# Kernel tuning notes

Hardware: AMD Instinct MI355X
Metric: run time of the kernel (lower is better)

## Reference

```python
import jax, jax.numpy as jnp
import numpy as np

EMBED_DIM = 768
NUM_HEADS = 12
HEAD_DIM = EMBED_DIM // NUM_HEADS
SCALE = HEAD_DIM ** -0.5


def setup_inputs() -> dict:
    key = jax.random.key(0)
    ks = jax.random.split(key, 5)
    B, T, D = 8, 1024, EMBED_DIM
    lim_qkv = (1.0 / D) ** 0.5
    x = jax.random.normal(ks[0], (B, T, D), dtype=jnp.float32)
    W_qkv = jax.random.uniform(ks[1], (D, 3 * D), dtype=jnp.float32, minval=-lim_qkv, maxval=lim_qkv)
    b_qkv = jax.random.uniform(ks[2], (3 * D,), dtype=jnp.float32, minval=-lim_qkv, maxval=lim_qkv)
    W_proj = jax.random.uniform(ks[3], (D, D), dtype=jnp.float32, minval=-lim_qkv, maxval=lim_qkv)
    b_proj = jax.random.uniform(ks[4], (D,), dtype=jnp.float32, minval=-lim_qkv, maxval=lim_qkv)
    return {"x": x, "W_qkv": W_qkv, "b_qkv": b_qkv, "W_proj": W_proj, "b_proj": b_proj}


def reference(x, W_qkv, b_qkv, W_proj, b_proj):
    B, T, D = x.shape
    H, Hd = NUM_HEADS, HEAD_DIM
    # fused QKV projection: [B,T,3D] -> [3,B,H,T,Hd]
    qkv = (x @ W_qkv + b_qkv).reshape(B, T, 3, H, Hd).transpose(2, 0, 3, 1, 4)
    q, k, v = qkv[0], qkv[1], qkv[2]
    attn = jax.nn.softmax(jnp.einsum("bhqd,bhkd->bhqk", q, k) * SCALE, axis=-1)
    out = jnp.einsum("bhqk,bhkd->bhqd", attn, v)  # [B,H,T,Hd]
    out = out.transpose(0, 2, 1, 3).reshape(B, T, D)
    return out @ W_proj + b_proj
```

## Files before the change

### kernel.cpp

```cpp
#include <hip/hip_runtime.h>
#include <hip/hip_bf16.h>
#include <stdint.h>

#define NB 8
#define NT 1024
#define ND 768
#define NH 12

static constexpr float QSCALE = 0.125f * 1.44269504f;

typedef __bf16 bf16x8 __attribute__((ext_vector_type(8)));
typedef float f32x4 __attribute__((ext_vector_type(4)));
typedef unsigned short u16;

__device__ __forceinline__ u16 f2b(float f) {
  union { float f; uint32_t u; } c; c.f = f;
  uint32_t u = c.u;
  u += 0x7fffu + ((u >> 16) & 1u);
  return (u16)(u >> 16);
}

__device__ __forceinline__ uint32_t pk2(float a, float b) {
  __hip_bfloat162 p = __float22bfloat162_rn(make_float2(a, b));
  return *reinterpret_cast<uint32_t*>(&p);
}

__device__ __forceinline__ float exp2_raw(float x) {
  float y;
  asm("v_exp_f32 %0, %1" : "=v"(y) : "v"(x));
  return y;
}

__device__ __forceinline__ void gload16(const void* g, void* l) {
  __builtin_amdgcn_global_load_lds(
      (const __attribute__((address_space(1))) void*)g,
      (__attribute__((address_space(3))) void*)l, 16, 0, 0);
}

__global__ void k_cast(const float* __restrict__ in, u16* __restrict__ out, int n4) {
  int i = blockIdx.x * blockDim.x + threadIdx.x;
  if (i >= n4) return;
  float4 v = reinterpret_cast<const float4*>(in)[i];
  ushort4 o;
  o.x = f2b(v.x); o.y = f2b(v.y); o.z = f2b(v.z); o.w = f2b(v.w);
  reinterpret_cast<ushort4*>(out)[i] = o;
}

__global__ void k_tcast(const float* __restrict__ in, u16* __restrict__ out, int R, int C) {
  __shared__ float tile[32][33];
  int c0 = blockIdx.x * 32, r0 = blockIdx.y * 32;
  int tx = threadIdx.x & 31, ty = threadIdx.x >> 5;
  #pragma unroll
  for (int rr = ty; rr < 32; rr += 8)
    tile[rr][tx] = in[(size_t)(r0 + rr) * C + c0 + tx];
  __syncthreads();
  #pragma unroll
  for (int cc = ty; cc < 32; cc += 8)
    out[(size_t)(c0 + cc) * R + r0 + tx] = f2b(tile[tx][cc]);
}

__launch_bounds__(256, 4)
__global__ void k_gemm_qkv(const u16* __restrict__ A, const u16* __restrict__ Bt,
                           const float* __restrict__ bias,
                           u16* __restrict__ Qg, u16* __restrict__ KV)
{
  __shared__ u16 Al[128 * 64];
  __shared__ u16 Bl[128 * 64];
  const int tid = threadIdx.x, lane = tid & 63, wv = tid >> 6;
  const int g = lane >> 4, r = lane & 15;
  const int wm = (wv >> 1) * 64, wn = (wv & 1) * 64;
  const int bid = blockIdx.x + blockIdx.y * 18;
  const int swz = (bid & 7) * 144 + (bid >> 3);
  const int m0 = (swz / 18) * 128, n0 = (swz % 18) * 128;
  const int srow = lane >> 3;
  const int scolsw = ((lane & 7) ^ (lane >> 3)) * 8;
  f32x4 acc[4][4] = {};
  for (int k0 = 0; k0 < ND; k0 += 64) {
    __syncthreads();
    #pragma unroll
    for (int i = 0; i < 4; ++i) {
      int c = wv * 4 + i;
      gload16(&A[(size_t)(m0 + c * 8 + srow) * ND + k0 + scolsw], &Al[c * 512]);
      gload16(&Bt[(size_t)(n0 + c * 8 + srow) * ND + k0 + scolsw], &Bl[c * 512]);
    }
    __syncthreads();
    #pragma unroll
    for (int kk = 0; kk < 2; ++kk) {
      bf16x8 af[4], bfr[4];
      #pragma unroll
      for (int mf = 0; mf < 4; ++mf)
        af[mf] = *reinterpret_cast<const bf16x8*>(
            &Al[(wm + mf * 16 + r) * 64 + (((kk << 2) + g) ^ (r & 7)) * 8]);
      #pragma unroll
      for (int nf = 0; nf < 4; ++nf)
        bfr[nf] = *reinterpret_cast<const bf16x8*>(
            &Bl[(wn + nf * 16 + r) * 64 + (((kk << 2) + g) ^ (r & 7)) * 8]);
      #pragma unroll
      for (int mf = 0; mf < 4; ++mf)
        #pragma unroll
        for (int nf = 0; nf < 4; ++nf)
          acc[mf][nf] = __builtin_amdgcn_mfma_f32_16x16x32_bf16(af[mf], bfr[nf], acc[mf][nf], 0, 0, 0);
    }
  }
  #pragma unroll
  for (int mf = 0; mf < 4; ++mf)
    #pragma unroll
    for (int nf = 0; nf < 4; ++nf) {
      int col = n0 + wn + nf * 16 + r;
      int which = col / ND, c = col - which * ND;
      int h = c >> 6, hd = c & 63;
      int row0 = m0 + wm + mf * 16 + 4 * g;
      int bb = row0 >> 10, t0 = row0 & 1023;
      size_t bh = (size_t)bb * NH + h;
      float b = bias[col];
      if (which == 0) {
        #pragma unroll
        for (int jj = 0; jj < 4; ++jj)
          Qg[(bh * NT + t0 + jj) * 64 + hd] = f2b((acc[mf][nf][jj] + b) * QSCALE);
      } else if (which == 1) {
        int kt = t0 >> 6, nfk = (t0 >> 4) & 3, rk0 = t0 & 15;
        int kk = hd >> 5, ghd = (hd >> 3) & 3, e = hd & 7;
        size_t base = (bh * 16 + kt) * 8192 + (size_t)(nfk * 2 + kk) * 512 + e;
        #pragma unroll
        for (int jj = 0; jj < 4; ++jj)
          KV[base + (ghd * 16 + rk0 + jj) * 8] = f2b(acc[mf][nf][jj] + b);
      } else {
        int kt = t0 >> 6, tl0 = t0 & 63;
        int ks = tl0 >> 5, gv = (tl0 >> 3) & 3, e0 = tl0 & 7;
        int hf = hd >> 4, rv = hd & 15;
        size_t base = (bh * 16 + kt) * 8192 + 4096 +
                      (size_t)(hf * 2 + ks) * 512 + (gv * 16 + rv) * 8 + e0;
        ushort4 o;
        o.x = f2b(acc[mf][nf][0] + b);
        o.y = f2b(acc[mf][nf][1] + b);
        o.z = f2b(acc[mf][nf][2] + b);
        o.w = f2b(acc[mf][nf][3] + b);
        *reinterpret_cast<ushort4*>(&KV[base]) = o;
      }
    }
}

__launch_bounds__(256, 4)
__global__ void k_attn(const u16* __restrict__ Qg, const u16* __restrict__ KV,
                       u16* __restrict__ Ob)
{
  __shared__ u16 kv[2][8192];
  __shared__ u16 Pl[4][1024];
  const int tid = threadIdx.x, lane = tid & 63, wv = tid >> 6;
  const int g = lane >> 4, r = lane & 15;
  const int bh = blockIdx.x;
  const int qt = blockIdx.y;
  const int bb = bh / NH, h = bh - bb * NH;
  const u16* Qb = Qg + (size_t)bh * NT * 64;
  const u16* kvb = KV + (size_t)bh * 16 * 8192;

  bf16x8 qf[2][2];
  #pragma unroll
  for (int mf = 0; mf < 2; ++mf)
    #pragma unroll
    for (int kk = 0; kk < 2; ++kk) {
      int qrow = qt * 128 + wv * 32 + mf * 16 + r;
      qf[mf][kk] = *reinterpret_cast<const bf16x8*>(&Qb[(size_t)qrow * 64 + kk * 32 + g * 8]);
    }

  bf16x8 ones;
  #pragma unroll
  for (int i = 0; i < 8; ++i) ones[i] = (__bf16)1.0f;

  f32x4 lacc[2] = {};
  f32x4 oacc[2][4] = {};

  const u16* srcbase = kvb + wv * 512 + lane * 8;
  #pragma unroll
  for (int i = 0; i < 4; ++i)
    gload16(srcbase + i * 2048, &kv[0][wv * 512 + i * 2048]);
  asm volatile("s_waitcnt vmcnt(0)" ::: "memory");
  __syncthreads();

  for (int kt = 0; kt < 16; ++kt) {
    const int cur = kt & 1;
    if (kt < 15) {
      const u16* src = srcbase + (size_t)(kt + 1) * 8192;
      #pragma unroll
      for (int i = 0; i < 4; ++i)
        gload16(src + i * 2048, &kv[cur ^ 1][wv * 512 + i * 2048]);
    }
    const u16* Kb = kv[cur];
    const u16* Vb = kv[cur] + 4096;
    u16* Pw = Pl[wv];

    f32x4 st[2][4] = {};
    __builtin_amdgcn_s_setprio(1);
    #pragma unroll
    for (int kk = 0; kk < 2; ++kk) {
      bf16x8 kf[4];
      #pragma unroll
      for (int nf = 0; nf < 4; ++nf)
        kf[nf] = *reinterpret_cast<const bf16x8*>(&Kb[(nf * 2 + kk) * 512 + lane * 8]);
      #pragma unroll
      for (int mf = 0; mf < 2; ++mf)
        #pragma unroll
        for (int nf = 0; nf < 4; ++nf)
          st[mf][nf] = __builtin_amdgcn_mfma_f32_16x16x32_bf16(kf[nf], qf[mf][kk], st[mf][nf], 0, 0, 0);
    }
    __builtin_amdgcn_s_setprio(0);

    #pragma unroll
    for (int mf = 0; mf < 2; ++mf)
      #pragma unroll
      for (int nf = 0; nf < 4; ++nf)
        #pragma unroll
        for (int jj = 0; jj < 4; ++jj)
          st[mf][nf][jj] = exp2_raw(st[mf][nf][jj]);

    #pragma unroll
    for (int ks = 0; ks < 2; ++ks) {
      #pragma unroll
      for (int mf = 0; mf < 2; ++mf)
        #pragma unroll
        for (int u = 0; u < 2; ++u) {
          uint2 w;
          w.x = pk2(st[mf][2 * ks + u][0], st[mf][2 * ks + u][1]);
          w.y = pk2(st[mf][2 * ks + u][2], st[mf][2 * ks + u][3]);
          int gp = u * 2 + (g >> 1);
          *reinterpret_cast<uint2*>(&Pw[mf * 512 + (gp * 16 + r) * 8 + (g & 1) * 4]) = w;
        }
      bf16x8 pf[2], vf[4];
      #pragma unroll
      for (int mf = 0; mf < 2; ++mf)
        pf[mf] = *reinterpret_cast<const bf16x8*>(&Pw[mf * 512 + lane * 8]);
      #pragma unroll
      for (int hf = 0; hf < 4; ++hf)
        vf[hf] = *reinterpret_cast<const bf16x8*>(&Vb[(hf * 2 + ks) * 512 + lane * 8]);
      __builtin_amdgcn_s_setprio(1);
      #pragma unroll
      for (int mf = 0; mf < 2; ++mf) {
        #pragma unroll
        for (int hf = 0; hf < 4; ++hf)
          oacc[mf][hf] = __builtin_amdgcn_mfma_f32_16x16x32_bf16(vf[hf], pf[mf], oacc[mf][hf], 0, 0, 0);
        lacc[mf] = __builtin_amdgcn_mfma_f32_16x16x32_bf16(ones, pf[mf], lacc[mf], 0, 0, 0);
      }
      __builtin_amdgcn_s_setprio(0);
    }

    asm volatile("s_waitcnt vmcnt(0)" ::: "memory");
    __syncthreads();
  }

  #pragma unroll
  for (int mf = 0; mf < 2; ++mf) {
    float inv = 1.f / lacc[mf][0];
    int row = qt * 128 + wv * 32 + mf * 16 + r;
    #pragma unroll
    for (int hf = 0; hf < 4; ++hf) {
      uint2 w;
      w.x = pk2(oacc[mf][hf][0] * inv, oacc[mf][hf][1] * inv);
      w.y = pk2(oacc[mf][hf][2] * inv, oacc[mf][hf][3] * inv);
      *reinterpret_cast<uint2*>(&Ob[((size_t)(bb * NT + row)) * ND + h * 64 + hf * 16 + 4 * g]) = w;
    }
  }
}

__launch_bounds__(256, 4)
__global__ void k_gemm_proj(const u16* __restrict__ A, const u16* __restrict__ Bt,
                            const float* __restrict__ bias, float* __restrict__ out)
{
  __shared__ u16 Al[128 * 32];
  __shared__ u16 Bl[64 * 32];
  const int tid = threadIdx.x, lane = tid & 63, wv = tid >> 6;
  const int g = lane >> 4, r = lane & 15;
  const int wm = (wv >> 1) * 64, wn = (wv & 1) * 32;
  const int bid = blockIdx.x + blockIdx.y * 12;
  const int swz = (bid & 7) * 96 + (bid >> 3);
  const int m0 = (swz / 12) * 128, n0 = (swz % 12) * 64;
  const int srow = lane >> 2;
  const int scol = (lane & 3) * 8;
  f32x4 acc[4][2] = {};
  for (int k0 = 0; k0 < ND; k0 += 32) {
    __syncthreads();
    #pragma unroll
    for (int i = 0; i < 2; ++i) {
      int c = wv * 2 + i;
      gload16(&A[(size_t)(m0 + c * 16 + srow) * ND + k0 + scol], &Al[c * 512]);
    }
    gload16(&Bt[(size_t)(n0 + wv * 16 + srow) * ND + k0 + scol], &Bl[wv * 512]);
    __syncthreads();
    bf16x8 af[4], bfr[2];
    #pragma unroll
    for (int mf = 0; mf < 4; ++mf)
      af[mf] = *reinterpret_cast<const bf16x8*>(&Al[(wm + mf * 16 + r) * 32 + g * 8]);
    #pragma unroll
    for (int nf = 0; nf < 2; ++nf)
      bfr[nf] = *reinterpret_cast<const bf16x8*>(&Bl[(wn + nf * 16 + r) * 32 + g * 8]);
    #pragma unroll
    for (int mf = 0; mf < 4; ++mf)
      #pragma unroll
      for (int nf = 0; nf < 2; ++nf)
        acc[mf][nf] = __builtin_amdgcn_mfma_f32_16x16x32_bf16(af[mf], bfr[nf], acc[mf][nf], 0, 0, 0);
  }
  #pragma unroll
  for (int mf = 0; mf < 4; ++mf)
    #pragma unroll
    for (int nf = 0; nf < 2; ++nf) {
      int col = n0 + wn + nf * 16 + r;
      float b = bias[col];
      #pragma unroll
      for (int jj = 0; jj < 4; ++jj) {
        int row = m0 + wm + mf * 16 + 4 * g + jj;
        out[(size_t)row * ND + col] = acc[mf][nf][jj] + b;
      }
    }
}

extern "C" void kernel_launch(void* const* d_in, const int* in_sizes, int n_in,
                              void* d_out, int out_size, void* d_ws, size_t ws_size,
                              hipStream_t stream)
{
  const float* x     = (const float*)d_in[0];
  const float* Wqkv  = (const float*)d_in[1];
  const float* bqkv  = (const float*)d_in[2];
  const float* Wproj = (const float*)d_in[3];
  const float* bproj = (const float*)d_in[4];
  float* out = (float*)d_out;

  char* ws = (char*)d_ws;
  u16* xb  = (u16*)(ws + 0);
  u16* wqt = (u16*)(ws + 12582912);
  u16* wpt = (u16*)(ws + 16121856);
  u16* Qg  = (u16*)(ws + 17301504);
  u16* KV  = (u16*)(ws + 29884416);
  u16* Ob  = (u16*)(ws + 55050240);

  k_cast<<<dim3((8192 * 768 / 4 + 255) / 256), dim3(256), 0, stream>>>(x, xb, 8192 * 768 / 4);
  k_tcast<<<dim3(2304 / 32, 768 / 32), dim3(256), 0, stream>>>(Wqkv, wqt, 768, 2304);
  k_tcast<<<dim3(768 / 32, 768 / 32), dim3(256), 0, stream>>>(Wproj, wpt, 768, 768);
  k_gemm_qkv<<<dim3(2304 / 128, 8192 / 128), dim3(256), 0, stream>>>(xb, wqt, bqkv, Qg, KV);
  k_attn<<<dim3(96, 8), dim3(256), 0, stream>>>(Qg, KV, Ob);
  k_gemm_proj<<<dim3(768 / 64, 8192 / 128), dim3(256), 0, stream>>>(Ob, wpt, bproj, out);
}
```

Baseline: 111.1 us.

## Use 256x256 double-buffered tiles with prefetch in QKV GEMM

The QKV GEMM moves to 512-thread blocks computing 256x256 output tiles, with LDS double buffering so the next K-slice loads while MFMAs run on the current one. Wave priority is raised around the MFMA blocks. The intent is more data reuse per LDS load and hiding global load latency behind compute. The cost is a large LDS footprint and one block per CU, which reduces latency hiding across blocks.

Result: slower. 132.2 us (+19.0%).

```diff
diff --git a/kernel.cpp b/kernel.cpp
--- a/kernel.cpp
+++ b/kernel.cpp
@@ -59,71 +59,104 @@
     out[(size_t)(c0 + cc) * R + r0 + tx] = f2b(tile[tx][cc]);
 }
 
-__launch_bounds__(256, 4)
+__launch_bounds__(512, 1)
 __global__ void k_gemm_qkv(const u16* __restrict__ A, const u16* __restrict__ Bt,
                            const float* __restrict__ bias,
                            u16* __restrict__ Qg, u16* __restrict__ KV)
 {
-  __shared__ u16 Al[128 * 64];
-  __shared__ u16 Bl[128 * 64];
+  __shared__ u16 Al[2][2][8192];
+  __shared__ u16 Bl[2][2][8192];
   const int tid = threadIdx.x, lane = tid & 63, wv = tid >> 6;
   const int g = lane >> 4, r = lane & 15;
-  const int wm = (wv >> 1) * 64, wn = (wv & 1) * 64;
-  const int bid = blockIdx.x + blockIdx.y * 18;
-  const int swz = (bid & 7) * 144 + (bid >> 3);
-  const int m0 = (swz / 18) * 128, n0 = (swz % 18) * 128;
+  const int ah = wv >> 2;
+  const int bq = wv & 3;
+  const int bhl = bq >> 1, bo = (bq & 1) * 64;
+  const int bid = blockIdx.x + blockIdx.y * 9;
+  const int swz = (bid & 7) * 36 + (bid >> 3);
+  const int m0 = (swz / 9) * 256, n0 = (swz % 9) * 256;
   const int srow = lane >> 3;
   const int scolsw = ((lane & 7) ^ (lane >> 3)) * 8;
-  f32x4 acc[4][4] = {};
-  for (int k0 = 0; k0 < ND; k0 += 64) {
-    __syncthreads();
-    #pragma unroll
-    for (int i = 0; i < 4; ++i) {
-      int c = wv * 4 + i;
-      gload16(&A[(size_t)(m0 + c * 8 + srow) * ND + k0 + scolsw], &Al[c * 512]);
-      gload16(&Bt[(size_t)(n0 + c * 8 + srow) * ND + k0 + scolsw], &Bl[c * 512]);
-    }
-    __syncthreads();
-    #pragma unroll
-    for (int kk = 0; kk < 2; ++kk) {
-      bf16x8 af[4], bfr[4];
-      #pragma unroll
-      for (int mf = 0; mf < 4; ++mf)
-        af[mf] = *reinterpret_cast<const bf16x8*>(
-            &Al[(wm + mf * 16 + r) * 64 + (((kk << 2) + g) ^ (r & 7)) * 8]);
-      #pragma unroll
-      for (int nf = 0; nf < 4; ++nf)
-        bfr[nf] = *reinterpret_cast<const bf16x8*>(
-            &Bl[(wn + nf * 16 + r) * 64 + (((kk << 2) + g) ^ (r & 7)) * 8]);
-      #pragma unroll
-      for (int mf = 0; mf < 4; ++mf)
-        #pragma unroll
-        for (int nf = 0; nf < 4; ++nf)
-          acc[mf][nf] = __builtin_amdgcn_mfma_f32_16x16x32_bf16(af[mf], bfr[nf], acc[mf][nf], 0, 0, 0);
-    }
+  const int c0 = wv * 2, c1 = wv * 2 + 1;
+
+  #define STG(G, rowbase, k0, dst)                                                      \
+    do {                                                                                \
+      gload16(&(G)[(size_t)((rowbase) + c0 * 8 + srow) * ND + (k0) + scolsw], &(dst)[c0 * 512]); \
+      gload16(&(G)[(size_t)((rowbase) + c1 * 8 + srow) * ND + (k0) + scolsw], &(dst)[c1 * 512]); \
+    } while (0)
+
+  f32x4 acc[8][4] = {};
+
+  STG(A, m0, 0, Al[0][0]);        STG(Bt, n0, 0, Bl[0][0]);
+  STG(A, m0 + 128, 0, Al[0][1]);  STG(Bt, n0 + 128, 0, Bl[0][1]);
+  STG(A, m0, 64, Al[1][0]);       STG(Bt, n0, 64, Bl[1][0]);
+  STG(A, m0 + 128, 64, Al[1][1]); STG(Bt, n0 + 128, 64, Bl[1][1]);
+  asm volatile("s_waitcnt vmcnt(8)" ::: "memory");
+  __builtin_amdgcn_s_barrier();
+
+  for (int t = 0; t < 12; ++t) {
+    const int kb = t & 1;
+    if (t >= 1 && t <= 10) {
+      const int nb = kb ^ 1;
+      const int k1 = (t + 1) * 64;
+      STG(A, m0, k1, Al[nb][0]);        STG(Bt, n0, k1, Bl[nb][0]);
+      STG(A, m0 + 128, k1, Al[nb][1]);  STG(Bt, n0 + 128, k1, Bl[nb][1]);
+    }
+    const u16* Ah = Al[kb][ah];
+    const u16* Bh = Bl[kb][bhl];
+    #pragma unroll
+    for (int p = 0; p < 4; ++p) {
+      const int mh = p & 1, nh = p >> 1;
+      bf16x8 af[4][2], bfr[2][2];
+      #pragma unroll
+      for (int kk = 0; kk < 2; ++kk) {
+        #pragma unroll
+        for (int q = 0; q < 4; ++q)
+          af[q][kk] = *reinterpret_cast<const bf16x8*>(
+              &Ah[(mh * 64 + q * 16 + r) * 64 + (((kk << 2) + g) ^ (r & 7)) * 8]);
+        #pragma unroll
+        for (int u = 0; u < 2; ++u)
+          bfr[u][kk] = *reinterpret_cast<const bf16x8*>(
+              &Bh[(bo + (nh * 2 + u) * 16 + r) * 64 + (((kk << 2) + g) ^ (r & 7)) * 8]);
+      }
+      __builtin_amdgcn_s_setprio(1);
+      #pragma unroll
+      for (int kk = 0; kk < 2; ++kk)
+        #pragma unroll
+        for (int q = 0; q < 4; ++q)
+          #pragma unroll
+          for (int u = 0; u < 2; ++u)
+            acc[mh * 4 + q][nh * 2 + u] = __builtin_amdgcn_mfma_f32_16x16x32_bf16(
+                af[q][kk], bfr[u][kk], acc[mh * 4 + q][nh * 2 + u], 0, 0, 0);
+      __builtin_amdgcn_s_setprio(0);
+    }
+    asm volatile("s_waitcnt lgkmcnt(0)" ::: "memory");
+    asm volatile("s_waitcnt vmcnt(0)" ::: "memory");
+    __builtin_amdgcn_s_barrier();
   }
-  #pragma unroll
-  for (int mf = 0; mf < 4; ++mf)
+  #undef STG
+
+  #pragma unroll
+  for (int amf = 0; amf < 8; ++amf)
     #pragma unroll
     for (int nf = 0; nf < 4; ++nf) {
-      int col = n0 + wn + nf * 16 + r;
+      int col = n0 + bq * 64 + nf * 16 + r;
       int which = col / ND, c = col - which * ND;
       int h = c >> 6, hd = c & 63;
-      int row0 = m0 + wm + mf * 16 + 4 * g;
+      int row0 = m0 + ah * 128 + amf * 16 + 4 * g;
       int bb = row0 >> 10, t0 = row0 & 1023;
       size_t bh = (size_t)bb * NH + h;
       float b = bias[col];
       if (which == 0) {
         #pragma unroll
         for (int jj = 0; jj < 4; ++jj)
-          Qg[(bh * NT + t0 + jj) * 64 + hd] = f2b((acc[mf][nf][jj] + b) * QSCALE);
+          Qg[(bh * NT + t0 + jj) * 64 + hd] = f2b((acc[amf][nf][jj] + b) * QSCALE);
       } else if (which == 1) {
         int kt = t0 >> 6, nfk = (t0 >> 4) & 3, rk0 = t0 & 15;
         int kk = hd >> 5, ghd = (hd >> 3) & 3, e = hd & 7;
         size_t base = (bh * 16 + kt) * 8192 + (size_t)(nfk * 2 + kk) * 512 + e;
         #pragma unroll
         for (int jj = 0; jj < 4; ++jj)
-          KV[base + (ghd * 16 + rk0 + jj) * 8] = f2b(acc[mf][nf][jj] + b);
+          KV[base + (ghd * 16 + rk0 + jj) * 8] = f2b(acc[amf][nf][jj] + b);
       } else {
         int kt = t0 >> 6, tl0 = t0 & 63;
         int ks = tl0 >> 5, gv = (tl0 >> 3) & 3, e0 = tl0 & 7;
@@ -131,10 +164,10 @@
         size_t base = (bh * 16 + kt) * 8192 + 4096 +
                       (size_t)(hf * 2 + ks) * 512 + (gv * 16 + rv) * 8 + e0;
         ushort4 o;
-        o.x = f2b(acc[mf][nf][0] + b);
-        o.y = f2b(acc[mf][nf][1] + b);
-        o.z = f2b(acc[mf][nf][2] + b);
-        o.w = f2b(acc[mf][nf][3] + b);
+        o.x = f2b(acc[amf][nf][0] + b);
+        o.y = f2b(acc[amf][nf][1] + b);
+        o.z = f2b(acc[amf][nf][2] + b);
+        o.w = f2b(acc[amf][nf][3] + b);
         *reinterpret_cast<ushort4*>(&KV[base]) = o;
       }
     }
@@ -334,7 +367,7 @@
   k_cast<<<dim3((8192 * 768 / 4 + 255) / 256), dim3(256), 0, stream>>>(x, xb, 8192 * 768 / 4);
   k_tcast<<<dim3(2304 / 32, 768 / 32), dim3(256), 0, stream>>>(Wqkv, wqt, 768, 2304);
   k_tcast<<<dim3(768 / 32, 768 / 32), dim3(256), 0, stream>>>(Wproj, wpt, 768, 768);
-  k_gemm_qkv<<<dim3(2304 / 128, 8192 / 128), dim3(256), 0, stream>>>(xb, wqt, bqkv, Qg, KV);
+  k_gemm_qkv<<<dim3(9, 32), dim3(512), 0, stream>>>(xb, wqt, bqkv, Qg, KV);
   k_attn<<<dim3(96, 8), dim3(256), 0, stream>>>(Qg, KV, Ob);
   k_gemm_proj<<<dim3(768 / 64, 8192 / 128), dim3(256), 0, stream>>>(Ob, wpt, bproj, out);
 }
```

## Load K/V fragments directly from global memory instead of LDS double buffering

Applied to the files above, without the earlier changes.

The attention kernel drops the shared-memory double-buffered K/V staging and its per-tile barriers. Each wave now reads its K and V MFMA fragments straight from global memory (relying on L2/L1 hits since the data is pre-swizzled), and all K fragments for a tile are loaded up front. This removes the LDS traffic and __syncthreads cost and may raise occupancy through lower LDS use. In exchange, the four waves redundantly fetch the same K/V tile from global memory and there is no explicit prefetch, so load latency may be exposed.

After: 110.0 us. About the same (-1.0%).

```diff
diff --git a/kernel.cpp b/kernel.cpp
--- a/kernel.cpp
+++ b/kernel.cpp
@@ -144,7 +144,6 @@
 __global__ void k_attn(const u16* __restrict__ Qg, const u16* __restrict__ KV,
                        u16* __restrict__ Ob)
 {
-  __shared__ u16 kv[2][8192];
   __shared__ u16 Pl[4][1024];
   const int tid = threadIdx.x, lane = tid & 63, wv = tid >> 6;
   const int g = lane >> 4, r = lane & 15;
@@ -169,40 +168,27 @@
 
   f32x4 lacc[2] = {};
   f32x4 oacc[2][4] = {};
-
-  const u16* srcbase = kvb + wv * 512 + lane * 8;
-  #pragma unroll
-  for (int i = 0; i < 4; ++i)
-    gload16(srcbase + i * 2048, &kv[0][wv * 512 + i * 2048]);
-  asm volatile("s_waitcnt vmcnt(0)" ::: "memory");
-  __syncthreads();
+  u16* Pw = Pl[wv];
 
   for (int kt = 0; kt < 16; ++kt) {
-    const int cur = kt & 1;
-    if (kt < 15) {
-      const u16* src = srcbase + (size_t)(kt + 1) * 8192;
-      #pragma unroll
-      for (int i = 0; i < 4; ++i)
-        gload16(src + i * 2048, &kv[cur ^ 1][wv * 512 + i * 2048]);
-    }
-    const u16* Kb = kv[cur];
-    const u16* Vb = kv[cur] + 4096;
-    u16* Pw = Pl[wv];
+    const u16* Kt = kvb + (size_t)kt * 8192;
+    const u16* Vt = Kt + 4096;
 
     f32x4 st[2][4] = {};
+    bf16x8 kf[4][2];
+    #pragma unroll
+    for (int nf = 0; nf < 4; ++nf)
+      #pragma unroll
+      for (int kk = 0; kk < 2; ++kk)
+        kf[nf][kk] = *reinterpret_cast<const bf16x8*>(&Kt[(nf * 2 + kk) * 512 + lane * 8]);
     __builtin_amdgcn_s_setprio(1);
     #pragma unroll
-    for (int kk = 0; kk < 2; ++kk) {
-      bf16x8 kf[4];
-      #pragma unroll
-      for (int nf = 0; nf < 4; ++nf)
-        kf[nf] = *reinterpret_cast<const bf16x8*>(&Kb[(nf * 2 + kk) * 512 + lane * 8]);
+    for (int kk = 0; kk < 2; ++kk)
       #pragma unroll
       for (int mf = 0; mf < 2; ++mf)
         #pragma unroll
         for (int nf = 0; nf < 4; ++nf)
-          st[mf][nf] = __builtin_amdgcn_mfma_f32_16x16x32_bf16(kf[nf], qf[mf][kk], st[mf][nf], 0, 0, 0);
-    }
+          st[mf][nf] = __builtin_amdgcn_mfma_f32_16x16x32_bf16(kf[nf][kk], qf[mf][kk], st[mf][nf], 0, 0, 0);
     __builtin_amdgcn_s_setprio(0);
 
     #pragma unroll
@@ -231,7 +217,7 @@
         pf[mf] = *reinterpret_cast<const bf16x8*>(&Pw[mf * 512 + lane * 8]);
       #pragma unroll
       for (int hf = 0; hf < 4; ++hf)
-        vf[hf] = *reinterpret_cast<const bf16x8*>(&Vb[(hf * 2 + ks) * 512 + lane * 8]);
+        vf[hf] = *reinterpret_cast<const bf16x8*>(&Vt[(hf * 2 + ks) * 512 + lane * 8]);
       __builtin_amdgcn_s_setprio(1);
       #pragma unroll
       for (int mf = 0; mf < 2; ++mf) {
@@ -242,9 +228,6 @@
       }
       __builtin_amdgcn_s_setprio(0);
     }
-
-    asm volatile("s_waitcnt vmcnt(0)" ::: "memory");
-    __syncthreads();
   }
 
   #pragma unroll
```
